# Optimization experiments

Measured on AMD Instinct MI355X. Metric: run time of the kernel, lower is better.

## Reference

```python
import jax, jax.numpy as jnp
import numpy as np

B, C, H, W = 16, 256, 64, 64
CI = 128  # inter_channels = in_channels // 2
BN_EPS = 1e-5


def conv1x1(x, w, b):
    # x: [B,C,H,W], w: [O,C], b: [O] -> [B,O,H,W]
    return jnp.einsum('bchw,oc->bohw', x, w) + b[None, :, None, None]


def maxpool2(x):
    # 2x2 max pool, stride 2
    b, c, h, w = x.shape
    return x.reshape(b, c, h // 2, 2, w // 2, 2).max(axis=(3, 5))


def setup_inputs() -> dict:
    key = jax.random.key(0)
    ks = jax.random.split(key, 13)
    s = 0.05
    return {
        'x': jax.random.normal(ks[0], (B, C, H, W), dtype=jnp.float32),
        'g_w': jax.random.normal(ks[1], (CI, C), dtype=jnp.float32) * s,
        'g_b': jax.random.normal(ks[2], (CI,), dtype=jnp.float32) * s,
        'theta_w': jax.random.normal(ks[3], (CI, C), dtype=jnp.float32) * s,
        'theta_b': jax.random.normal(ks[4], (CI,), dtype=jnp.float32) * s,
        'phi_w': jax.random.normal(ks[5], (CI, C), dtype=jnp.float32) * s,
        'phi_b': jax.random.normal(ks[6], (CI,), dtype=jnp.float32) * s,
        'W_w': jax.random.normal(ks[7], (C, CI), dtype=jnp.float32) * s,
        'W_b': jax.random.normal(ks[8], (C,), dtype=jnp.float32) * s,
        # BN in eval mode; gamma/beta randomized (the original inits them to 0,
        # which would zero out the whole branch) so the reference is non-trivial.
        'bn_gamma': jax.random.normal(ks[9], (C,), dtype=jnp.float32) * s,
        'bn_beta': jax.random.normal(ks[10], (C,), dtype=jnp.float32) * s,
        'bn_mean': jnp.zeros((C,), dtype=jnp.float32),
        'bn_var': jnp.ones((C,), dtype=jnp.float32),
    }


def reference(x, g_w, g_b, theta_w, theta_b, phi_w, phi_b, W_w, W_b,
              bn_gamma, bn_beta, bn_mean, bn_var):
    b, c, h, w = x.shape
    ci = g_w.shape[0]
    # g and phi are subsampled (2x2 maxpool); theta is full resolution
    g_x = maxpool2(conv1x1(x, g_w, g_b)).reshape(b, ci, -1)            # [B,CI,Nk]
    g_x = jnp.transpose(g_x, (0, 2, 1))                                 # [B,Nk,CI]
    theta_x = conv1x1(x, theta_w, theta_b).reshape(b, ci, -1)           # [B,CI,N]
    theta_x = jnp.transpose(theta_x, (0, 2, 1))                         # [B,N,CI]
    phi_x = maxpool2(conv1x1(x, phi_w, phi_b)).reshape(b, ci, -1)       # [B,CI,Nk]
    f = jnp.matmul(theta_x, phi_x)                                      # [B,N,Nk]
    f_div_C = jax.nn.softmax(f, axis=-1)
    y = jnp.matmul(f_div_C, g_x)                                        # [B,N,CI]
    y = jnp.transpose(y, (0, 2, 1)).reshape(b, ci, h, w)                # [B,CI,H,W]
    # W: 1x1 conv back to C channels + BatchNorm (eval mode)
    w_y = conv1x1(y, W_w, W_b)
    inv = jax.lax.rsqrt(bn_var + BN_EPS)
    w_y = (w_y - bn_mean[None, :, None, None]) * (bn_gamma * inv)[None, :, None, None] \
          + bn_beta[None, :, None, None]
    return w_y + x
```

## Files before the change

kernel.cpp:

```cpp
#include <hip/hip_runtime.h>
#include <hip/hip_bf16.h>

#define BB  16
#define CC  256
#define NN  4096
#define CI  128
#define NK  1024

typedef __attribute__((ext_vector_type(4))) float f32x4;
typedef __attribute__((ext_vector_type(16))) float f32x16;
typedef __attribute__((ext_vector_type(8))) short bf16x8;

__device__ __forceinline__ unsigned short f2b(float f) {
  union { float f; unsigned u; } v; v.f = f;
  unsigned r = v.u + 0x7fffu + ((v.u >> 16) & 1u);
  return (unsigned short)(r >> 16);
}
__device__ __forceinline__ float b2f(unsigned short u) {
  union { unsigned u; float f; } v; v.u = ((unsigned)u) << 16;
  return v.f;
}
__device__ __forceinline__ unsigned cvtpk(float lo, float hi) {
  unsigned r;
  asm volatile("v_cvt_pk_bf16_f32 %0, %1, %2" : "=v"(r) : "v"(lo), "v"(hi));
  return r;
}

__global__ __launch_bounds__(256) void k0_prep(
    const float* __restrict__ gw,  const float* __restrict__ gb,
    const float* __restrict__ tw,  const float* __restrict__ tb,
    const float* __restrict__ pw,  const float* __restrict__ pb,
    const float* __restrict__ Ww,  const float* __restrict__ Wb,
    const float* __restrict__ gam, const float* __restrict__ bet,
    const float* __restrict__ mea, const float* __restrict__ var,
    unsigned short* __restrict__ wpk,
    unsigned short* __restrict__ wWpk,
    float* __restrict__ biases)
{
  int i = blockIdx.x * 256 + threadIdx.x;
  if (i < 98304) {
    int mat  = i >> 15;
    int o    = i & 32767;
    int frag = o >> 9;
    int lane = (o >> 3) & 63;
    int j    = o & 7;
    int wn   = frag >> 4, nt = (frag >> 3) & 1, k0s = frag & 7;
    int row  = wn * 32 + nt * 16 + (lane & 15);
    int col  = k0s * 32 + (lane >> 4) * 8 + j;
    const float* src = (mat == 0) ? tw : ((mat == 1) ? pw : gw);
    wpk[i] = f2b(src[row * 256 + col]);
  }
  else if (i < 131072) {
    int o2   = i - 98304;
    int oc   = o2 >> 12;
    int kc   = (o2 >> 9) & 7;
    int lane = (o2 >> 3) & 63;
    int j    = o2 & 7;
    int orow = oc * 32 + (lane & 31);
    int ci   = kc * 16 + (lane >> 5) * 8 + j;
    wWpk[o2] = f2b(Ww[orow * 128 + ci]);
  }
  else {
    int j = i - 131072;
    if (j < 128)       biases[j] = tb[j];
    else if (j < 256)  biases[j] = pb[j - 128];
    else if (j < 384)  biases[j] = gb[j - 256];
    else if (j < 640) { int o = j - 384; biases[j] = gam[o] * rsqrtf(var[o] + 1e-5f); }
    else if (j < 896) { int o = j - 640; float A = gam[o] * rsqrtf(var[o] + 1e-5f);
                        biases[j] = (Wb[o] - mea[o]) * A + bet[o]; }
  }
}

__device__ __forceinline__ int xswz(int s, int cb) {
  return s * 256 + ((cb ^ ((s >> 2) & 7) ^ ((s & 1) << 2)) << 3);
}

__global__ __launch_bounds__(512, 2) void k1_qkv(
    const float* __restrict__ x,
    const unsigned short* __restrict__ wpk,
    const float* __restrict__ biases,
    unsigned short* __restrict__ thq,
    unsigned short* __restrict__ phit,
    unsigned short* __restrict__ gt)
{
  __shared__ __align__(16) unsigned short lds[128 * 256];
  const int tid = threadIdx.x;
  const int hp = blockIdx.x;
  const int b  = blockIdx.y;
  const int s0 = hp * 128;
  const int wave = tid >> 6, lane = tid & 63, lr = lane & 15, lg = lane >> 4;
  const int wm = wave >> 2, wn = wave & 3;

  const float* xb = x + (size_t)b * CC * NN + s0;
  const int sg4 = (tid & 31) * 4;

#define LOADG(V, IT) { const int ch = ((tid >> 5) + (IT) * 16) * 4;            \
    V[0] = *(const f32x4*)&xb[(size_t)(ch + 0) * NN + sg4];                    \
    V[1] = *(const f32x4*)&xb[(size_t)(ch + 1) * NN + sg4];                    \
    V[2] = *(const f32x4*)&xb[(size_t)(ch + 2) * NN + sg4];                    \
    V[3] = *(const f32x4*)&xb[(size_t)(ch + 3) * NN + sg4]; }
#define WRITEG(V, IT) { const int ch = ((tid >> 5) + (IT) * 16) * 4;           \
    _Pragma("unroll")                                                          \
    for (int j = 0; j < 4; ++j) {                                              \
      int s = sg4 + j;                                                         \
      unsigned d0 = cvtpk(V[0][j], V[1][j]);                                   \
      unsigned d1 = cvtpk(V[2][j], V[3][j]);                                   \
      unsigned long long d = ((unsigned long long)d1 << 32) | (unsigned long long)d0; \
      *(unsigned long long*)&lds[xswz(s, ch >> 3) + (ch & 7)] = d; } }

  {
    f32x4 v0[4], v1[4];
    LOADG(v0, 0);
    LOADG(v1, 1); WRITEG(v0, 0);
    LOADG(v0, 2); WRITEG(v1, 1);
    LOADG(v1, 3); WRITEG(v0, 2);
    WRITEG(v1, 3);
  }
#undef LOADG
#undef WRITEG
  __syncthreads();

  const int ci_nt0 = wn * 32 + lr;
  const float* bias_all = biases;
  const unsigned short* wbase = wpk + (size_t)wn * 8192 + (size_t)lane * 8;

#pragma unroll
  for (int mat = 0; mat < 3; ++mat) {
    const unsigned short* wmat = wbase + mat * 32768;
    f32x4 acc[4][2];
    f32x4 z = {0.f, 0.f, 0.f, 0.f};
#pragma unroll
    for (int mt = 0; mt < 4; ++mt) { acc[mt][0] = z; acc[mt][1] = z; }

#pragma unroll
    for (int k0s = 0; k0s < 8; ++k0s) {
      bf16x8 a[4];
#pragma unroll
      for (int mt = 0; mt < 4; ++mt) {
        int s = (mt >> 1) * 64 + wm * 32 + (mt & 1) * 16 + lr;
        a[mt] = *(const bf16x8*)&lds[xswz(s, k0s * 4 + lg)];
      }
#pragma unroll
      for (int nt = 0; nt < 2; ++nt) {
        bf16x8 bw = *(const bf16x8*)&wmat[(nt * 8 + k0s) * 512];
#pragma unroll
        for (int mt = 0; mt < 4; ++mt)
          acc[mt][nt] = __builtin_amdgcn_mfma_f32_16x16x32_bf16(a[mt], bw, acc[mt][nt], 0, 0, 0);
      }
    }

    float bv0 = bias_all[mat * 128 + ci_nt0];
    float bv1 = bias_all[mat * 128 + ci_nt0 + 16];

    if (mat == 0) {
      unsigned short* tq = thq + ((size_t)b * NN + s0) * CI;
#pragma unroll
      for (int mt = 0; mt < 4; ++mt) {
        int sb = (mt >> 1) * 64 + wm * 32 + (mt & 1) * 16 + lg * 4;
#pragma unroll
        for (int nt = 0; nt < 2; ++nt) {
          float bv = nt ? bv1 : bv0;
          int ci = ci_nt0 + nt * 16;
#pragma unroll
          for (int r = 0; r < 4; ++r)
            tq[(size_t)(sb + r) * CI + ci] = f2b(acc[mt][nt][r] + bv);
        }
      }
    } else if (mat == 1) {
      unsigned short* ph = phit + ((size_t)b * NK + hp * 32) * CI;
#pragma unroll
      for (int mt = 0; mt < 2; ++mt) {
#pragma unroll
        for (int nt = 0; nt < 2; ++nt) {
          float bv = nt ? bv1 : bv0;
          int ci = ci_nt0 + nt * 16;
#pragma unroll
          for (int p = 0; p < 2; ++p) {
            float vmx = fmaxf(fmaxf(acc[mt][nt][2 * p], acc[mt][nt][2 * p + 1]),
                              fmaxf(acc[mt + 2][nt][2 * p], acc[mt + 2][nt][2 * p + 1]));
            int kv = wm * 16 + mt * 8 + lg * 2 + p;
            ph[(size_t)kv * CI + ci] = f2b(vmx + bv);
          }
        }
      }
    } else {
      unsigned short* gg = gt + (size_t)b * CI * NK + hp * 32;
#pragma unroll
      for (int mt = 0; mt < 2; ++mt) {
#pragma unroll
        for (int nt = 0; nt < 2; ++nt) {
          float bv = nt ? bv1 : bv0;
          int ci = ci_nt0 + nt * 16;
          unsigned short e[2];
#pragma unroll
          for (int p = 0; p < 2; ++p) {
            float vmx = fmaxf(fmaxf(acc[mt][nt][2 * p], acc[mt][nt][2 * p + 1]),
                              fmaxf(acc[mt + 2][nt][2 * p], acc[mt + 2][nt][2 * p + 1]));
            e[p] = f2b(vmx + bv);
          }
          unsigned pk = (unsigned)e[0] | ((unsigned)e[1] << 16);
          int kv = wm * 16 + mt * 8 + lg * 2;
          *(unsigned*)&gg[(size_t)ci * NK + kv] = pk;
        }
      }
    }
  }
}

__global__ __launch_bounds__(256, 2) void k2_attn(
    const unsigned short* __restrict__ thq,
    const unsigned short* __restrict__ phit,
    const unsigned short* __restrict__ gt,
    const unsigned short* __restrict__ wWpk,
    const float* __restrict__ biases,
    const float* __restrict__ x,
    float* __restrict__ out)
{
  __shared__ __align__(16) unsigned short Kt[2][64 * 128];
  __shared__ __align__(16) unsigned short Vt[2][128 * 64];
  const int tid = threadIdx.x;
  const int b = blockIdx.y;
  const int wave = tid >> 6, lane = tid & 63;
  const int l31 = lane & 31, hi = lane >> 5;
  const int q0 = blockIdx.x * 128 + wave * 32;

  const unsigned short* phB = phit + (size_t)b * NK * CI;
  const unsigned short* gB  = gt + (size_t)b * CI * NK;

  bf16x8 qf[8];
#pragma unroll
  for (int ks = 0; ks < 8; ++ks)
    qf[ks] = *(const bf16x8*)&thq[((size_t)b * NN + q0 + l31) * CI + ks * 16 + hi * 8];

  f32x16 oac[4];
#pragma unroll
  for (int nt = 0; nt < 4; ++nt)
#pragma unroll
    for (int r = 0; r < 16; ++r) oac[nt][r] = 0.f;
  float ls[4];
#pragma unroll
  for (int i = 0; i < 4; ++i) ls[i] = 0.f;

  const int skv = tid >> 4;
  const int scb = tid & 15;
  const int sci = tid >> 3;
  const int skb = tid & 7;

  bf16x8 kreg[4], vreg[4];
#pragma unroll
  for (int i = 0; i < 4; ++i) {
    kreg[i] = *(const bf16x8*)&phB[(size_t)(i * 16 + skv) * CI + scb * 8];
    vreg[i] = *(const bf16x8*)&gB[(size_t)(i * 32 + sci) * NK + skb * 8];
  }
#pragma unroll
  for (int i = 0; i < 4; ++i) {
    int kv = i * 16 + skv;
    *(bf16x8*)&Kt[0][kv * 128 + ((scb ^ (kv & 7)) << 3)] = kreg[i];
    int ci = i * 32 + sci;
    *(bf16x8*)&Vt[0][ci * 64 + ((skb ^ (ci & 7)) << 3)] = vreg[i];
  }
  __syncthreads();
#pragma unroll
  for (int i = 0; i < 4; ++i) {
    kreg[i] = *(const bf16x8*)&phB[(size_t)(64 + i * 16 + skv) * CI + scb * 8];
    vreg[i] = *(const bf16x8*)&gB[(size_t)(i * 32 + sci) * NK + 64 + skb * 8];
  }

  for (int kt = 0; kt < 16; ++kt) {
    const unsigned short* KtP = &Kt[kt & 1][0];
    const unsigned short* VtP = &Vt[kt & 1][0];

    bf16x8 pa[4];
#pragma unroll
    for (int nt = 0; nt < 2; ++nt) {
      f32x16 sacc;
#pragma unroll
      for (int r = 0; r < 16; ++r) sacc[r] = 0.f;
      const int kv = nt * 32 + l31;
      __builtin_amdgcn_s_setprio(1);
#pragma unroll
      for (int ks = 0; ks < 8; ++ks) {
        bf16x8 kf = *(const bf16x8*)&KtP[kv * 128 + ((((ks << 1) + hi) ^ (kv & 7)) << 3)];
        sacc = __builtin_amdgcn_mfma_f32_32x32x16_bf16(kf, qf[ks], sacc, 0, 0, 0);
      }
      __builtin_amdgcn_s_setprio(0);

#pragma unroll
      for (int h = 0; h < 2; ++h) {
        float e[8];
#pragma unroll
        for (int j = 0; j < 8; ++j) e[j] = __expf(sacc[h * 8 + j] - 20.f);
        ls[nt * 2 + h] += ((e[0] + e[1]) + (e[2] + e[3])) + ((e[4] + e[5]) + (e[6] + e[7]));
        unsigned pkA = cvtpk(e[0], e[1]);
        unsigned pkB = cvtpk(e[2], e[3]);
        unsigned pkC = cvtpk(e[4], e[5]);
        unsigned pkD = cvtpk(e[6], e[7]);
        unsigned sendA = hi ? pkA : pkC;
        unsigned sendB = hi ? pkB : pkD;
        unsigned recvA = (unsigned)__shfl_xor((int)sendA, 32);
        unsigned recvB = (unsigned)__shfl_xor((int)sendB, 32);
        union { unsigned u[4]; bf16x8 v; } pu;
        pu.u[0] = hi ? recvA : pkA;
        pu.u[1] = hi ? recvB : pkB;
        pu.u[2] = hi ? pkC : recvA;
        pu.u[3] = hi ? pkD : recvB;
        pa[nt * 2 + h] = pu.v;
      }
    }

    __builtin_amdgcn_s_setprio(1);
#pragma unroll
    for (int ks = 0; ks < 4; ++ks) {
#pragma unroll
      for (int nt = 0; nt < 4; ++nt) {
        int ci = nt * 32 + l31;
        bf16x8 vf = *(const bf16x8*)&VtP[ci * 64 + ((((ks << 1) + hi) ^ (ci & 7)) << 3)];
        oac[nt] = __builtin_amdgcn_mfma_f32_32x32x16_bf16(vf, pa[ks], oac[nt], 0, 0, 0);
      }
    }
    __builtin_amdgcn_s_setprio(0);

    if (kt < 15) {
      unsigned short* KtW = &Kt[(kt + 1) & 1][0];
      unsigned short* VtW = &Vt[(kt + 1) & 1][0];
#pragma unroll
      for (int i = 0; i < 4; ++i) {
        int kv = i * 16 + skv;
        *(bf16x8*)&KtW[kv * 128 + ((scb ^ (kv & 7)) << 3)] = kreg[i];
        int ci = i * 32 + sci;
        *(bf16x8*)&VtW[ci * 64 + ((skb ^ (ci & 7)) << 3)] = vreg[i];
      }
      __syncthreads();
      if (kt < 14) {
        int kv0n = (kt + 2) * 64;
#pragma unroll
        for (int i = 0; i < 4; ++i) {
          kreg[i] = *(const bf16x8*)&phB[(size_t)(kv0n + i * 16 + skv) * CI + scb * 8];
          vreg[i] = *(const bf16x8*)&gB[(size_t)(i * 32 + sci) * NK + kv0n + skb * 8];
        }
      }
    }
  }

  float lsum = (ls[0] + ls[1]) + (ls[2] + ls[3]);
  float ltot = lsum + __shfl_xor(lsum, 32);
  float linv = 1.f / ltot;

  bf16x8 yb[8];
#pragma unroll
  for (int nt = 0; nt < 4; ++nt) {
#pragma unroll
    for (int h = 0; h < 2; ++h) {
      float v[8];
#pragma unroll
      for (int j = 0; j < 8; ++j) v[j] = oac[nt][h * 8 + j] * linv;
      unsigned pkA = cvtpk(v[0], v[1]);
      unsigned pkB = cvtpk(v[2], v[3]);
      unsigned pkC = cvtpk(v[4], v[5]);
      unsigned pkD = cvtpk(v[6], v[7]);
      unsigned sendA = hi ? pkA : pkC;
      unsigned sendB = hi ? pkB : pkD;
      unsigned recvA = (unsigned)__shfl_xor((int)sendA, 32);
      unsigned recvB = (unsigned)__shfl_xor((int)sendB, 32);
      union { unsigned u[4]; bf16x8 v8; } pu;
      pu.u[0] = hi ? recvA : pkA;
      pu.u[1] = hi ? recvB : pkB;
      pu.u[2] = hi ? pkC : recvA;
      pu.u[3] = hi ? pkD : recvB;
      yb[nt * 2 + h] = pu.v8;
    }
  }

  const float* Ao = biases + 384;
  const float* Bo = biases + 640;
  const float* xq = x + (size_t)b * CC * NN + q0 + l31;
  float* oq = out + (size_t)b * CC * NN + q0 + l31;
#pragma unroll
  for (int oc = 0; oc < 8; ++oc) {
    f32x16 d2;
#pragma unroll
    for (int r = 0; r < 16; ++r) d2[r] = 0.f;
#pragma unroll
    for (int kc = 0; kc < 8; ++kc) {
      bf16x8 wf = *(const bf16x8*)&wWpk[(size_t)(oc * 8 + kc) * 512 + lane * 8];
      d2 = __builtin_amdgcn_mfma_f32_32x32x16_bf16(wf, yb[kc], d2, 0, 0, 0);
    }
#pragma unroll
    for (int r = 0; r < 16; ++r) {
      int o = oc * 32 + (r & 3) + 8 * (r >> 2) + 4 * hi;
      float res = d2[r] * Ao[o] + Bo[o] + xq[(size_t)o * NN];
      oq[(size_t)o * NN] = res;
    }
  }
}

extern "C" void kernel_launch(void* const* d_in, const int* in_sizes, int n_in,
                              void* d_out, int out_size, void* d_ws, size_t ws_size,
                              hipStream_t stream) {
  const float* x   = (const float*)d_in[0];
  const float* gw  = (const float*)d_in[1];
  const float* gb  = (const float*)d_in[2];
  const float* tw  = (const float*)d_in[3];
  const float* tb  = (const float*)d_in[4];
  const float* pw  = (const float*)d_in[5];
  const float* pb  = (const float*)d_in[6];
  const float* Ww  = (const float*)d_in[7];
  const float* Wb  = (const float*)d_in[8];
  const float* gam = (const float*)d_in[9];
  const float* bet = (const float*)d_in[10];
  const float* mea = (const float*)d_in[11];
  const float* var = (const float*)d_in[12];

  char* ws = (char*)d_ws;
  unsigned short* wpk  = (unsigned short*)(ws);
  unsigned short* wWpk = (unsigned short*)(ws + 196608);
  float*          bias = (float*)(ws + 262144);
  unsigned short* thq  = (unsigned short*)(ws + 266240);
  unsigned short* phit = (unsigned short*)(ws + 266240 + 16777216);
  unsigned short* gt   = (unsigned short*)(ws + 266240 + 16777216 + 4194304);
  float* out = (float*)d_out;

  k0_prep<<<516, 256, 0, stream>>>(gw, gb, tw, tb, pw, pb, Ww, Wb, gam, bet, mea, var,
                                   wpk, wWpk, bias);
  k1_qkv<<<dim3(32, 16), 512, 0, stream>>>(x, wpk, bias, thq, phit, gt);
  k2_attn<<<dim3(32, 16), 256, 0, stream>>>(thq, phit, gt, wWpk, bias, x, out);
}
```

Measured before the change: 94.77 us.

## Single-buffer K/V tiles in attention kernel to raise occupancy to three blocks

Replaces the double-buffered K/V LDS tiles and the register prefetch pipeline with a single buffer that is loaded synchronously at the start of each KV tile, with barriers before and after the load. Launch bounds are raised from 2 to 3 blocks per CU. Halving the LDS footprint and dropping the prefetch registers is meant to let more waves hide memory latency. In exchange, each iteration now stalls on global loads with no software overlap, and the register budget per thread shrinks, which risks spilling.

```diff
diff --git a/kernel.cpp b/kernel.cpp
--- a/kernel.cpp
+++ b/kernel.cpp
@@ -207,7 +207,7 @@
   }
 }
 
-__global__ __launch_bounds__(256, 2) void k2_attn(
+__global__ __launch_bounds__(256, 3) void k2_attn(
     const unsigned short* __restrict__ thq,
     const unsigned short* __restrict__ phit,
     const unsigned short* __restrict__ gt,
@@ -216,8 +216,8 @@
     const float* __restrict__ x,
     float* __restrict__ out)
 {
-  __shared__ __align__(16) unsigned short Kt[2][64 * 128];
-  __shared__ __align__(16) unsigned short Vt[2][128 * 64];
+  __shared__ __align__(16) unsigned short Kt[64 * 128];
+  __shared__ __align__(16) unsigned short Vt[128 * 64];
   const int tid = threadIdx.x;
   const int b = blockIdx.y;
   const int wave = tid >> 6, lane = tid & 63;
@@ -246,29 +246,25 @@
   const int sci = tid >> 3;
   const int skb = tid & 7;
 
-  bf16x8 kreg[4], vreg[4];
-#pragma unroll
-  for (int i = 0; i < 4; ++i) {
-    kreg[i] = *(const bf16x8*)&phB[(size_t)(i * 16 + skv) * CI + scb * 8];
-    vreg[i] = *(const bf16x8*)&gB[(size_t)(i * 32 + sci) * NK + skb * 8];
-  }
-#pragma unroll
-  for (int i = 0; i < 4; ++i) {
-    int kv = i * 16 + skv;
-    *(bf16x8*)&Kt[0][kv * 128 + ((scb ^ (kv & 7)) << 3)] = kreg[i];
-    int ci = i * 32 + sci;
-    *(bf16x8*)&Vt[0][ci * 64 + ((skb ^ (ci & 7)) << 3)] = vreg[i];
-  }
-  __syncthreads();
-#pragma unroll
-  for (int i = 0; i < 4; ++i) {
-    kreg[i] = *(const bf16x8*)&phB[(size_t)(64 + i * 16 + skv) * CI + scb * 8];
-    vreg[i] = *(const bf16x8*)&gB[(size_t)(i * 32 + sci) * NK + 64 + skb * 8];
-  }
-
   for (int kt = 0; kt < 16; ++kt) {
-    const unsigned short* KtP = &Kt[kt & 1][0];
-    const unsigned short* VtP = &Vt[kt & 1][0];
+    const int kv0 = kt * 64;
+    __syncthreads();
+    {
+      bf16x8 kreg[4], vreg[4];
+#pragma unroll
+      for (int i = 0; i < 4; ++i) {
+        kreg[i] = *(const bf16x8*)&phB[(size_t)(kv0 + i * 16 + skv) * CI + scb * 8];
+        vreg[i] = *(const bf16x8*)&gB[(size_t)(i * 32 + sci) * NK + kv0 + skb * 8];
+      }
+#pragma unroll
+      for (int i = 0; i < 4; ++i) {
+        int kv = i * 16 + skv;
+        *(bf16x8*)&Kt[kv * 128 + ((scb ^ (kv & 7)) << 3)] = kreg[i];
+        int ci = i * 32 + sci;
+        *(bf16x8*)&Vt[ci * 64 + ((skb ^ (ci & 7)) << 3)] = vreg[i];
+      }
+    }
+    __syncthreads();
 
     bf16x8 pa[4];
 #pragma unroll
@@ -280,7 +276,7 @@
       __builtin_amdgcn_s_setprio(1);
 #pragma unroll
       for (int ks = 0; ks < 8; ++ks) {
-        bf16x8 kf = *(const bf16x8*)&KtP[kv * 128 + ((((ks << 1) + hi) ^ (kv & 7)) << 3)];
+        bf16x8 kf = *(const bf16x8*)&Kt[kv * 128 + ((((ks << 1) + hi) ^ (kv & 7)) << 3)];
         sacc = __builtin_amdgcn_mfma_f32_32x32x16_bf16(kf, qf[ks], sacc, 0, 0, 0);
       }
       __builtin_amdgcn_s_setprio(0);
@@ -314,32 +310,11 @@
 #pragma unroll
       for (int nt = 0; nt < 4; ++nt) {
         int ci = nt * 32 + l31;
-        bf16x8 vf = *(const bf16x8*)&VtP[ci * 64 + ((((ks << 1) + hi) ^ (ci & 7)) << 3)];
+        bf16x8 vf = *(const bf16x8*)&Vt[ci * 64 + ((((ks << 1) + hi) ^ (ci & 7)) << 3)];
         oac[nt] = __builtin_amdgcn_mfma_f32_32x32x16_bf16(vf, pa[ks], oac[nt], 0, 0, 0);
       }
     }
     __builtin_amdgcn_s_setprio(0);
-
-    if (kt < 15) {
-      unsigned short* KtW = &Kt[(kt + 1) & 1][0];
-      unsigned short* VtW = &Vt[(kt + 1) & 1][0];
-#pragma unroll
-      for (int i = 0; i < 4; ++i) {
-        int kv = i * 16 + skv;
-        *(bf16x8*)&KtW[kv * 128 + ((scb ^ (kv & 7)) << 3)] = kreg[i];
-        int ci = i * 32 + sci;
-        *(bf16x8*)&VtW[ci * 64 + ((skb ^ (ci & 7)) << 3)] = vreg[i];
-      }
-      __syncthreads();
-      if (kt < 14) {
-        int kv0n = (kt + 2) * 64;
-#pragma unroll
-        for (int i = 0; i < 4; ++i) {
-          kreg[i] = *(const bf16x8*)&phB[(size_t)(kv0n + i * 16 + skv) * CI + scb * 8];
-          vreg[i] = *(const bf16x8*)&gB[(size_t)(i * 32 + sci) * NK + kv0n + skb * 8];
-        }
-      }
-    }
   }
 
   float lsum = (ls[0] + ls[1]) + (ls[2] + ls[3]);
```

Result: slower. 112.6 us (+18.8%).
